# Performance work log

Measured on AMD Instinct MI355X. Metric: run time of the kernel, lower is better.

Reference implementation:

```python
import jax, jax.numpy as jnp
import numpy as np

DIM, HEADS, DHEAD, CTX_DIM, FF_MULT = 320, 8, 40, 768, 4
INNER_FF = FF_MULT * DIM  # 1280
EPS = 1e-5


def layer_norm(x, g, b):
    mu = jnp.mean(x, axis=-1, keepdims=True)
    var = jnp.mean((x - mu) ** 2, axis=-1, keepdims=True)
    return (x - mu) * jax.lax.rsqrt(var + EPS) * g + b


def attention(x, ctx, wq, wk, wv, wo, bo):
    # x: [b, i, DIM], ctx: [b, j, c]
    b, i, _ = x.shape
    j = ctx.shape[1]
    q = (x @ wq).reshape(b, i, HEADS, DHEAD)
    k = (ctx @ wk).reshape(b, j, HEADS, DHEAD)
    v = (ctx @ wv).reshape(b, j, HEADS, DHEAD)
    scale = DHEAD ** -0.5
    sim = jnp.einsum('bihd,bjhd->bhij', q, k) * scale  # full NxN, non-flash
    attn = jax.nn.softmax(sim, axis=-1)
    out = jnp.einsum('bhij,bjhd->bihd', attn, v).reshape(b, i, HEADS * DHEAD)
    return out @ wo + bo


def setup_inputs() -> dict:
    key = jax.random.key(0)
    ks = jax.random.split(key, 24)
    nrm = lambda k, shp, fan: jax.random.normal(k, shp, jnp.float32) * (fan ** -0.5)
    d = {
        'x': jax.random.normal(ks[0], (1, 4096, DIM), jnp.float32),
        'context': jax.random.normal(ks[1], (1, 77, CTX_DIM), jnp.float32),
        'n1_g': jnp.ones((DIM,), jnp.float32), 'n1_b': jnp.zeros((DIM,), jnp.float32),
        'a1_wq': nrm(ks[2], (DIM, DIM), DIM), 'a1_wk': nrm(ks[3], (DIM, DIM), DIM),
        'a1_wv': nrm(ks[4], (DIM, DIM), DIM), 'a1_wo': nrm(ks[5], (DIM, DIM), DIM),
        'a1_bo': jnp.zeros((DIM,), jnp.float32),
        'n2_g': jnp.ones((DIM,), jnp.float32), 'n2_b': jnp.zeros((DIM,), jnp.float32),
        'a2_wq': nrm(ks[6], (DIM, DIM), DIM), 'a2_wk': nrm(ks[7], (CTX_DIM, DIM), CTX_DIM),
        'a2_wv': nrm(ks[8], (CTX_DIM, DIM), CTX_DIM), 'a2_wo': nrm(ks[9], (DIM, DIM), DIM),
        'a2_bo': jnp.zeros((DIM,), jnp.float32),
        'n3_g': jnp.ones((DIM,), jnp.float32), 'n3_b': jnp.zeros((DIM,), jnp.float32),
        'ff_w1': nrm(ks[10], (DIM, 2 * INNER_FF), DIM),
        'ff_b1': jnp.zeros((2 * INNER_FF,), jnp.float32),
        'ff_w2': nrm(ks[11], (INNER_FF, DIM), INNER_FF),
        'ff_b2': jnp.zeros((DIM,), jnp.float32),
    }
    return d


def reference(x, context, n1_g, n1_b, a1_wq, a1_wk, a1_wv, a1_wo, a1_bo,
              n2_g, n2_b, a2_wq, a2_wk, a2_wv, a2_wo, a2_bo,
              n3_g, n3_b, ff_w1, ff_b1, ff_w2, ff_b2):
    # self-attention
    x = attention(layer_norm(x, n1_g, n1_b), layer_norm(x, n1_g, n1_b),
                  a1_wq, a1_wk, a1_wv, a1_wo, a1_bo) + x
    # cross-attention with text context
    x = attention(layer_norm(x, n2_g, n2_b), context,
                  a2_wq, a2_wk, a2_wv, a2_wo, a2_bo) + x
    # GEGLU feed-forward
    h = layer_norm(x, n3_g, n3_b) @ ff_w1 + ff_b1
    val, gate = jnp.split(h, 2, axis=-1)
    x = (val * jax.nn.gelu(gate, approximate=False)) @ ff_w2 + ff_b2 + x
    return x
```

## Files before the change

### kernel.cpp

```cpp
#include <hip/hip_runtime.h>
#include <hip/hip_bf16.h>
#include <math.h>

typedef __bf16 bf16;
typedef __attribute__((ext_vector_type(8))) __bf16 bf16x8;
typedef __attribute__((ext_vector_type(4))) __bf16 bf16x4;
typedef __attribute__((ext_vector_type(4))) float f32x4;
typedef __attribute__((ext_vector_type(2))) float f32x2;
typedef __attribute__((ext_vector_type(4))) short shortx4;

#define NTOK 4096
#define DIM  320
#define HEADS 8
#define DHEAD 40
#define NCTX 77
#define CTXD 768
#define IFF  1280

#define QSCALE (0.15811388300841897f * 1.4426950408889634f)

__device__ __forceinline__ bf16x8 bzero8() {
    bf16x8 v;
#pragma unroll
    for (int e = 0; e < 8; ++e) v[e] = (bf16)0.0f;
    return v;
}

__device__ __forceinline__ void gld_lds16(const void* g, void* l) {
    __builtin_amdgcn_global_load_lds(
        (const __attribute__((address_space(1))) void*)g,
        (__attribute__((address_space(3))) void*)l, 16, 0, 0);
}

__device__ __forceinline__ void ln_body(const float* __restrict__ X, const float* __restrict__ g,
                                        const float* __restrict__ b, bf16* __restrict__ Y, int row) {
    int lane = threadIdx.x & 63;
    const float* xr = X + (size_t)row * DIM;
    float v[5];
    float sum = 0.f;
#pragma unroll
    for (int c = 0; c < 5; ++c) { v[c] = xr[c * 64 + lane]; sum += v[c]; }
#pragma unroll
    for (int off = 1; off < 64; off <<= 1) sum += __shfl_xor(sum, off);
    float mu = sum * (1.f / 320.f);
    float vs = 0.f;
#pragma unroll
    for (int c = 0; c < 5; ++c) { float d = v[c] - mu; vs += d * d; }
#pragma unroll
    for (int off = 1; off < 64; off <<= 1) vs += __shfl_xor(vs, off);
    float rs = rsqrtf(vs * (1.f / 320.f) + 1e-5f);
    bf16* yr = Y + (size_t)row * DIM;
#pragma unroll
    for (int c = 0; c < 5; ++c)
        yr[c * 64 + lane] = (bf16)((v[c] - mu) * rs * g[c * 64 + lane] + b[c * 64 + lane]);
}

__global__ __launch_bounds__(256)
void layernorm_kernel(const float* __restrict__ X, const float* __restrict__ g,
                      const float* __restrict__ b, bf16* __restrict__ Y) {
    ln_body(X, g, b, Y, blockIdx.x * 4 + (threadIdx.x >> 6));
}

#define PRE_TILES 2280
#define CONV_BLOCKS 231
#define LN1_BLOCKS 1024

struct PreJob { const float* src; bf16* dst; int K, N, ntx, tile0, perm; };
struct PreTab { PreJob j[10]; };

__global__ __launch_bounds__(256)
void preprocess_all(PreTab P, const float* __restrict__ ctx, bf16* __restrict__ ctxb,
                    const float* __restrict__ x, const float* __restrict__ n1_g,
                    const float* __restrict__ n1_b, bf16* __restrict__ lnbuf) {
    const int b = blockIdx.x;
    const int t = threadIdx.x;
    if (b >= PRE_TILES + CONV_BLOCKS) {
        ln_body(x, n1_g, n1_b, lnbuf, (b - PRE_TILES - CONV_BLOCKS) * 4 + (t >> 6));
        return;
    }
    if (b >= PRE_TILES) {
        int i = (b - PRE_TILES) * 256 + t;
        if (i < NCTX * CTXD) ctxb[i] = (bf16)ctx[i];
        return;
    }
    const int tx = t & 31, ty = t >> 5;
    int ji = 0;
#pragma unroll
    for (int k = 1; k < 10; ++k)
        if (b >= P.j[k].tile0) ji = k;
    const PreJob jb = P.j[ji];
    const int local = b - jb.tile0;
    const int n0 = (local % jb.ntx) * 32;
    const int k0 = (local / jb.ntx) * 32;

    __shared__ float tile[32][33];
#pragma unroll
    for (int i = 0; i < 4; ++i)
        tile[ty + i * 8][tx] = jb.src[(size_t)(k0 + ty + i * 8) * jb.N + n0 + tx];
    __syncthreads();
#pragma unroll
    for (int i = 0; i < 4; ++i) {
        int n = n0 + ty + i * 8;
        int nd = jb.perm ? ((n < 1280) ? 2 * n : 2 * (n - 1280) + 1) : n;
        jb.dst[(size_t)nd * jb.K + k0 + tx] = (bf16)tile[tx][ty + i * 8];
    }
}

template <int EPI, int BM, int BN, int SWZ>
__global__ __launch_bounds__(256)
void gemm_db(const bf16* __restrict__ A, const bf16* __restrict__ Bt,
             int M, int N, int K,
             bf16* __restrict__ Y0, bf16* __restrict__ Y1, bf16* __restrict__ Y2,
             float* Yf, const float* __restrict__ bias, const float* res, int trs) {
    constexpr int ABYTES = BM * 128;
    constexpr int BBYTES = BN * 128;
    constexpr int FB = ABYTES + BBYTES;
    constexpr int WM = BM / 2;
    constexpr int WN = BN / 2;
    constexpr int MI = WM / 16;
    constexpr int NI = WN / 16;
    constexpr int ACH = BM / 32;
    constexpr int BCH = BN / 32;
    __shared__ char smem[2 * FB];
    const int t = threadIdx.x, lane = t & 63, w = t >> 6;
    const int wr = w >> 1, wc = w & 1;

    int bx = blockIdx.x, by = blockIdx.y;
    if (SWZ) {
        int gx = gridDim.x;
        int nwg = gx * gridDim.y;
        int bid = by * gx + bx;
        int s = (bid & 7) * (nwg >> 3) + (bid >> 3);
        bx = s % gx; by = s / gx;
    }
    const int m0 = bx * BM;
    const int n0 = by * BN;

    const bf16* asrc[ACH];
    const bf16* bsrc[BCH];
#pragma unroll
    for (int i = 0; i < ACH; ++i) {
        int ch = i * 256 + t;
        int row = ch >> 3, seg = (ch & 7) ^ (row & 7);
        asrc[i] = A + (size_t)(m0 + row) * K + seg * 8;
    }
#pragma unroll
    for (int i = 0; i < BCH; ++i) {
        int ch = i * 256 + t;
        int row = ch >> 3, seg = (ch & 7) ^ (row & 7);
        bsrc[i] = Bt + (size_t)(n0 + row) * K + seg * 8;
    }

    f32x4 acc[MI][NI];
#pragma unroll
    for (int mi = 0; mi < MI; ++mi)
#pragma unroll
        for (int ni = 0; ni < NI; ++ni)
#pragma unroll
            for (int r = 0; r < 4; ++r) acc[mi][ni][r] = 0.f;

    auto STAGE = [&](char* base, int k0) {
#pragma unroll
        for (int i = 0; i < ACH; ++i)
            gld_lds16(asrc[i] + k0, base + (i * 256 + w * 64) * 16);
#pragma unroll
        for (int i = 0; i < BCH; ++i)
            gld_lds16(bsrc[i] + k0, base + ABYTES + (i * 256 + w * 64) * 16);
    };

    char* cur = smem;
    char* nxt = smem + FB;
    STAGE(cur, 0);
    __syncthreads();

    for (int k0 = 0; k0 < K; k0 += 64) {
        if (k0 + 64 < K) STAGE(nxt, k0 + 64);
        bf16x8 a[MI][2], b[NI][2];
#pragma unroll
        for (int mi = 0; mi < MI; ++mi)
#pragma unroll
            for (int kh = 0; kh < 2; ++kh) {
                int row = wr * WM + mi * 16 + (lane & 15);
                a[mi][kh] = *(const bf16x8*)(cur + row * 128 +
                             ((kh * 64 + (lane >> 4) * 16) ^ ((row & 7) << 4)));
            }
#pragma unroll
        for (int ni = 0; ni < NI; ++ni)
#pragma unroll
            for (int kh = 0; kh < 2; ++kh) {
                int row = wc * WN + ni * 16 + (lane & 15);
                b[ni][kh] = *(const bf16x8*)(cur + ABYTES + row * 128 +
                             ((kh * 64 + (lane >> 4) * 16) ^ ((row & 7) << 4)));
            }
#pragma unroll
        for (int mi = 0; mi < MI; ++mi)
#pragma unroll
            for (int ni = 0; ni < NI; ++ni) {
                acc[mi][ni] = __builtin_amdgcn_mfma_f32_16x16x32_bf16(a[mi][0], b[ni][0], acc[mi][ni], 0, 0, 0);
                acc[mi][ni] = __builtin_amdgcn_mfma_f32_16x16x32_bf16(a[mi][1], b[ni][1], acc[mi][ni], 0, 0, 0);
            }
        __syncthreads();
        char* tmp = cur; cur = nxt; nxt = tmp;
    }

#pragma unroll
    for (int mi = 0; mi < MI; ++mi)
#pragma unroll
        for (int ni = 0; ni < NI; ++ni) {
            const int col = n0 + wc * WN + ni * 16 + (lane & 15);
            const int rowb = m0 + wr * WM + mi * 16 + (lane >> 4) * 4;
            if (EPI == 5) {
                if (col < 320) {
#pragma unroll
                    for (int r = 0; r < 4; ++r)
                        Y0[(size_t)(rowb + r) * 320 + col] = (bf16)(acc[mi][ni][r] * QSCALE);
                } else if (col < 640) {
#pragma unroll
                    for (int r = 0; r < 4; ++r)
                        Y1[(size_t)(rowb + r) * 320 + (col - 320)] = (bf16)acc[mi][ni][r];
                } else {
                    bf16x4 tv;
#pragma unroll
                    for (int r = 0; r < 4; ++r) tv[r] = (bf16)acc[mi][ni][r];
                    *(bf16x4*)(Y2 + (size_t)(col - 640) * trs + rowb) = tv;
                }
            } else if (EPI == 7) {
                int bidx = (col & 1) ? (1280 + (col >> 1)) : (col >> 1);
                float bc = bias[bidx];
#pragma unroll
                for (int r = 0; r < 4; ++r) {
                    float v = acc[mi][ni][r] + bc;
                    float other = __shfl_xor(v, 1);
                    if (!(col & 1)) {
                        float gl = 0.5f * other * (1.f + erff(other * 0.70710678118654752f));
                        Y0[(size_t)(rowb + r) * 1280 + (col >> 1)] = (bf16)(v * gl);
                    }
                }
            } else {
#pragma unroll
                for (int r = 0; r < 4; ++r) {
                    int row = rowb + r;
                    if (row < M) {
                        float v = acc[mi][ni][r];
                        if (EPI == 4) Y0[(size_t)row * N + col] = (bf16)(v * QSCALE);
                        else Yf[(size_t)row * N + col] = v + bias[col] + res[(size_t)row * N + col];
                    }
                }
            }
        }
}

__global__ __launch_bounds__(256)
void ln2_plus_cross(const float* __restrict__ X, const float* __restrict__ g,
                    const float* __restrict__ bb, bf16* __restrict__ Y,
                    const bf16* __restrict__ A, const bf16* __restrict__ Bt,
                    bf16* __restrict__ Y0, bf16* __restrict__ Y2, int trs) {
    __shared__ char smem[24 * 1024];
    if (blockIdx.x < 1024) {
        ln_body(X, g, bb, Y, blockIdx.x * 4 + (threadIdx.x >> 6));
        return;
    }
    const int M = NCTX, K = CTXD;
    const int t = threadIdx.x;
    const int lane = t & 63;
    const int w = t >> 6;
    const int wr = w >> 1, wc = w & 1;
    const int n0 = (blockIdx.x - 1024) * 64;

    f32x4 acc[4][2];
#pragma unroll
    for (int mi = 0; mi < 4; ++mi)
#pragma unroll
        for (int ni = 0; ni < 2; ++ni)
#pragma unroll
            for (int r = 0; r < 4; ++r) acc[mi][ni][r] = 0.f;

    for (int k0 = 0; k0 < K; k0 += 64) {
#pragma unroll
        for (int i = 0; i < 4; ++i) {
            int c = t + i * 256;
            int row = c >> 3, seg = c & 7;
            bf16x8 v = bzero8();
            if (row < M) v = *(const bf16x8*)(A + (size_t)row * K + k0 + seg * 8);
            *(bf16x8*)(smem + row * 128 + ((seg * 16) ^ ((row & 7) << 4))) = v;
        }
#pragma unroll
        for (int i = 0; i < 2; ++i) {
            int c = t + i * 256;
            int row = c >> 3, seg = c & 7;
            bf16x8 v = *(const bf16x8*)(Bt + (size_t)(n0 + row) * K + k0 + seg * 8);
            *(bf16x8*)(smem + 16 * 1024 + row * 128 + ((seg * 16) ^ ((row & 7) << 4))) = v;
        }
        __syncthreads();

        bf16x8 a[4][2], bfr[2][2];
#pragma unroll
        for (int mi = 0; mi < 4; ++mi)
#pragma unroll
            for (int kh = 0; kh < 2; ++kh) {
                int row = wr * 64 + mi * 16 + (lane & 15);
                a[mi][kh] = *(const bf16x8*)(smem + row * 128 +
                             ((kh * 64 + (lane >> 4) * 16) ^ ((row & 7) << 4)));
            }
#pragma unroll
        for (int ni = 0; ni < 2; ++ni)
#pragma unroll
            for (int kh = 0; kh < 2; ++kh) {
                int row = wc * 32 + ni * 16 + (lane & 15);
                bfr[ni][kh] = *(const bf16x8*)(smem + 16 * 1024 + row * 128 +
                               ((kh * 64 + (lane >> 4) * 16) ^ ((row & 7) << 4)));
            }
#pragma unroll
        for (int mi = 0; mi < 4; ++mi)
#pragma unroll
            for (int ni = 0; ni < 2; ++ni) {
                acc[mi][ni] = __builtin_amdgcn_mfma_f32_16x16x32_bf16(a[mi][0], bfr[ni][0], acc[mi][ni], 0, 0, 0);
                acc[mi][ni] = __builtin_amdgcn_mfma_f32_16x16x32_bf16(a[mi][1], bfr[ni][1], acc[mi][ni], 0, 0, 0);
            }
        __syncthreads();
    }

#pragma unroll
    for (int mi = 0; mi < 4; ++mi)
#pragma unroll
        for (int ni = 0; ni < 2; ++ni) {
            const int col = n0 + wc * 32 + ni * 16 + (lane & 15);
            const int rowb = wr * 64 + mi * 16 + (lane >> 4) * 4;
            if (col < 320) {
#pragma unroll
                for (int r = 0; r < 4; ++r)
                    if (rowb + r < M) Y0[(size_t)(rowb + r) * 320 + col] = (bf16)acc[mi][ni][r];
            } else {
                bf16x4 tv;
#pragma unroll
                for (int r = 0; r < 4; ++r) tv[r] = (bf16)acc[mi][ni][r];
                *(bf16x4*)(Y2 + (size_t)(col - 320) * trs + rowb) = tv;
            }
        }
}

#define KVT 64
#define KBYTES 5120
#define VBYTES 6144
#define FBUF (KBYTES + VBYTES)

template <int DIRECT>
__global__ __launch_bounds__(256, 4)
void flash_attn9(const bf16* __restrict__ Qg, const bf16* __restrict__ Kg,
                 const bf16* __restrict__ VTg, bf16* __restrict__ O,
                 bf16* __restrict__ Opart, float* __restrict__ MLpart,
                 int nkv, int vstride, int tiles_per_split) {
    __shared__ char smem[2 * FBUF];
    const int t = threadIdx.x, lane = t & 63, w = t >> 6;
    const int g = lane >> 4, q = lane & 15;
    const int h = blockIdx.y, split = blockIdx.z;
    const int qb = blockIdx.x * 64 + w * 16;

    const int ntiles = (nkv + KVT - 1) / KVT;
    const int tt0 = split * tiles_per_split;
    int tt1 = tt0 + tiles_per_split;
    if (tt1 > ntiles) tt1 = ntiles;

    if (t < 128) {
        bf16x8 v = bzero8();
        if (((t & 63) >> 3) == 0) {
#pragma unroll
            for (int e = 0; e < 8; ++e) v[e] = (bf16)1.0f;
        }
        *(bf16x8*)(smem + (t >> 6) * FBUF + KBYTES + 5120 + (t & 63) * 16) = v;
    }

    const int nslot = (w == 3) ? 1 : 3;
    const bf16* srcp[3];
    int dstoff[3], sstep[3];
#pragma unroll
    for (int s = 0; s < 3; ++s) {
        int id = w * 3 + s;
        if (id < 5) {
            int c16 = id * 64 + lane;
            int row = c16 / 5, seg = c16 - row * 5;
            srcp[s] = Kg + (size_t)(tt0 * KVT + row) * DIM + h * DHEAD + seg * 8;
            sstep[s] = KVT * DIM;
            dstoff[s] = id * 1024;
        } else {
            int vv = id - 5;
            int c16 = vv * 64 + lane;
            int row = c16 >> 3, seg = (c16 & 7) ^ (row & 7);
            srcp[s] = VTg + (size_t)(h * DHEAD + row) * vstride + tt0 * KVT + seg * 8;
            sstep[s] = KVT;
            dstoff[s] = KBYTES + vv * 1024;
        }
    }

#define STAGE(BUFOFF)                                                     \
    do {                                                                  \
        _Pragma("unroll")                                                 \
        for (int s = 0; s < 3; ++s) {                                     \
            if (s < nslot) {                                              \
                gld_lds16(srcp[s], smem + (BUFOFF) + dstoff[s]);          \
                srcp[s] += sstep[s];                                      \
            }                                                             \
        }                                                                 \
    } while (0)

    bf16x8 qf0 = *(const bf16x8*)(Qg + (size_t)(qb + q) * DIM + h * DHEAD + g * 8);
    bf16x8 qf1 = bzero8();
    if (g == 0) qf1 = *(const bf16x8*)(Qg + (size_t)(qb + q) * DIM + h * DHEAD + 32);

    f32x4 accO[3];
#pragma unroll
    for (int dt = 0; dt < 3; ++dt)
#pragma unroll
        for (int r = 0; r < 4; ++r) accO[dt][r] = 0.f;
    float m_run = -1e30f;

    const int swv = (q & 7) << 4;

#define TILE_BODY(KSC, J0)                                                        \
    do {                                                                          \
        const char* Ks_ = (KSC);                                                  \
        const char* Vs_ = Ks_ + KBYTES;                                           \
        const char* kb0b = Ks_ + q * 80 + g * 16;                                 \
        const char* kb1b = Ks_ + q * 80 + 64;                                     \
        f32x4 s4[4];                                                              \
        __builtin_amdgcn_s_setprio(1);                                            \
        _Pragma("unroll")                                                         \
        for (int jt = 0; jt < 4; ++jt) {                                          \
            bf16x8 kb0 = *(const bf16x8*)(kb0b + jt * 1280);                      \
            bf16x8 kb1 = *(const bf16x8*)(kb1b + jt * 1280);                      \
            f32x4 z;                                                              \
            _Pragma("unroll") for (int r = 0; r < 4; ++r) z[r] = 0.f;             \
            z = __builtin_amdgcn_mfma_f32_16x16x32_bf16(kb0, qf0, z, 0, 0, 0);    \
            z = __builtin_amdgcn_mfma_f32_16x16x32_bf16(kb1, qf1, z, 0, 0, 0);    \
            s4[jt] = z;                                                           \
        }                                                                         \
        __builtin_amdgcn_s_setprio(0);                                            \
        if ((J0) + KVT > nkv) {                                                   \
            _Pragma("unroll") for (int jt = 0; jt < 4; ++jt)                      \
            _Pragma("unroll") for (int r = 0; r < 4; ++r)                         \
                if ((J0) + jt * 16 + g * 4 + r >= nkv) s4[jt][r] = -1e30f;        \
        }                                                                         \
        float mvv0 = fmaxf(fmaxf(fmaxf(s4[0][0], s4[1][0]), s4[2][0]), s4[3][0]); \
        float mvv1 = fmaxf(fmaxf(fmaxf(s4[0][1], s4[1][1]), s4[2][1]), s4[3][1]); \
        float mvv2 = fmaxf(fmaxf(fmaxf(s4[0][2], s4[1][2]), s4[2][2]), s4[3][2]); \
        float mvv3 = fmaxf(fmaxf(fmaxf(s4[0][3], s4[1][3]), s4[2][3]), s4[3][3]); \
        float mt = fmaxf(fmaxf(fmaxf(mvv0, mvv1), mvv2), mvv3);                   \
        mt = fmaxf(mt, __shfl_xor(mt, 16));                                       \
        mt = fmaxf(mt, __shfl_xor(mt, 32));                                       \
        if (!__all(mt <= m_run + 8.f)) {                                          \
            float mnew = fmaxf(m_run, mt);                                        \
            float f = exp2f(m_run - mnew);                                        \
            m_run = mnew;                                                         \
            _Pragma("unroll") for (int dt = 0; dt < 3; ++dt)                      \
            _Pragma("unroll") for (int r = 0; r < 4; ++r) accO[dt][r] *= f;       \
        }                                                                         \
        union PU { bf16x4 hv; shortx4 sv; } pk[4];                                \
        _Pragma("unroll") for (int jt = 0; jt < 4; ++jt) {                        \
            bf16x4 hv;                                                            \
            _Pragma("unroll") for (int r = 0; r < 4; ++r)                         \
                hv[r] = (bf16)exp2f(s4[jt][r] - m_run);                           \
            pk[jt].hv = hv;                                                       \
        }                                                                         \
        __builtin_amdgcn_s_setprio(1);                                            \
        const char* vqb = Vs_ + q * 128;                                          \
        _Pragma("unroll") for (int jt = 0; jt < 4; ++jt) {                        \
            const char* vj = vqb + ((jt * 32 + g * 8) ^ swv);                     \
            _Pragma("unroll") for (int dt = 0; dt < 3; ++dt) {                    \
                shortx4 vb = *(const shortx4*)(vj + dt * 2048);                   \
                accO[dt] = __builtin_amdgcn_mfma_f32_16x16x16bf16_1k(             \
                               vb, pk[jt].sv, accO[dt], 0, 0, 0);                 \
            }                                                                     \
        }                                                                         \
        __builtin_amdgcn_s_setprio(0);                                            \
        __syncthreads();                                                          \
    } while (0)

    STAGE(0);
    __syncthreads();

    int tt = tt0;
    while (tt < tt1) {
        if (tt + 1 < tt1) STAGE(FBUF);
        TILE_BODY(smem, tt * KVT);
        ++tt;
        if (tt >= tt1) break;
        if (tt + 1 < tt1) STAGE(0);
        TILE_BODY(smem + FBUF, tt * KVT);
        ++tt;
    }
#undef TILE_BODY
#undef STAGE

    float l = __shfl(accO[2][0], 32 + q);

    if (DIRECT) {
        float inv = 1.f / l;
#pragma unroll
        for (int dt = 0; dt < 3; ++dt) {
            if (dt < 2 || g < 2) {
                bf16x4 o;
#pragma unroll
                for (int r = 0; r < 4; ++r) o[r] = (bf16)(accO[dt][r] * inv);
                *(bf16x4*)(O + (size_t)(qb + q) * DIM + h * DHEAD + dt * 16 + g * 4) = o;
            }
        }
    } else {
        size_t rowi = (size_t)(split * HEADS + h) * NTOK + qb + q;
#pragma unroll
        for (int dt = 0; dt < 3; ++dt) {
            if (dt < 2 || g < 2) {
                bf16x4 o;
#pragma unroll
                for (int r = 0; r < 4; ++r) o[r] = (bf16)accO[dt][r];
                *(bf16x4*)(Opart + rowi * 40 + dt * 16 + g * 4) = o;
            }
        }
        if (g == 2) {
            f32x2 ml;
            ml[0] = m_run; ml[1] = accO[2][0];
            *(f32x2*)(MLpart + rowi * 2) = ml;
        }
    }
}

__global__ __launch_bounds__(256)
void flash_combine(const bf16* __restrict__ Opart, const float* __restrict__ MLpart,
                   bf16* __restrict__ O) {
    int idx = blockIdx.x * 256 + threadIdx.x;
    int qi = idx / 40, c = idx - qi * 40;
    int h = c / 5, c8 = c - h * 5;
    float mv[4], lv[4];
    float M = -1e30f;
#pragma unroll
    for (int s = 0; s < 4; ++s) {
        f32x2 ml = *(const f32x2*)(MLpart + ((size_t)(s * HEADS + h) * NTOK + qi) * 2);
        mv[s] = ml[0]; lv[s] = ml[1];
        M = fmaxf(M, ml[0]);
    }
    float wgt[4], denom = 0.f;
#pragma unroll
    for (int s = 0; s < 4; ++s) { wgt[s] = exp2f(mv[s] - M); denom += wgt[s] * lv[s]; }
    float inv = 1.f / denom;
    float o[8];
#pragma unroll
    for (int e = 0; e < 8; ++e) o[e] = 0.f;
#pragma unroll
    for (int s = 0; s < 4; ++s) {
        bf16x8 op = *(const bf16x8*)(Opart + ((size_t)(s * HEADS + h) * NTOK + qi) * 40 + c8 * 8);
#pragma unroll
        for (int e = 0; e < 8; ++e) o[e] += wgt[s] * (float)op[e];
    }
    bf16x8 ov;
#pragma unroll
    for (int e = 0; e < 8; ++e) ov[e] = (bf16)(o[e] * inv);
    *(bf16x8*)(O + (size_t)qi * DIM + h * DHEAD + c8 * 8) = ov;
}

extern "C" void kernel_launch(void* const* d_in, const int* in_sizes, int n_in,
                              void* d_out, int out_size, void* d_ws, size_t ws_size,
                              hipStream_t stream) {
    const float* x     = (const float*)d_in[0];
    const float* ctx   = (const float*)d_in[1];
    const float* n1_g  = (const float*)d_in[2];
    const float* n1_b  = (const float*)d_in[3];
    const float* a1_wq = (const float*)d_in[4];
    const float* a1_wk = (const float*)d_in[5];
    const float* a1_wv = (const float*)d_in[6];
    const float* a1_wo = (const float*)d_in[7];
    const float* a1_bo = (const float*)d_in[8];
    const float* n2_g  = (const float*)d_in[9];
    const float* n2_b  = (const float*)d_in[10];
    const float* a2_wq = (const float*)d_in[11];
    const float* a2_wk = (const float*)d_in[12];
    const float* a2_wv = (const float*)d_in[13];
    const float* a2_wo = (const float*)d_in[14];
    const float* a2_bo = (const float*)d_in[15];
    const float* n3_g  = (const float*)d_in[16];
    const float* n3_b  = (const float*)d_in[17];
    const float* ff_w1 = (const float*)d_in[18];
    const float* ff_b1 = (const float*)d_in[19];
    const float* ff_w2 = (const float*)d_in[20];
    const float* ff_b2 = (const float*)d_in[21];

    char* ws = (char*)d_ws;
    size_t off = 0;
    auto alloc = [&](size_t bytes) -> char* {
        char* p = ws + off;
        off += (bytes + 255) & ~(size_t)255;
        return p;
    };
    bf16* lnbuf  = (bf16*)alloc((size_t)NTOK * DIM * 2);
    bf16* qbuf   = (bf16*)alloc((size_t)NTOK * DIM * 2);
    bf16* kbuf   = (bf16*)alloc((size_t)NTOK * DIM * 2);
    bf16* vtbuf  = (bf16*)alloc((size_t)DIM * NTOK * 2);
    bf16* abuf   = (bf16*)alloc((size_t)NTOK * DIM * 2);
    bf16* hbuf   = (bf16*)alloc((size_t)NTOK * 2 * IFF * 2);
    bf16* gbuf   = (bf16*)alloc((size_t)NTOK * IFF * 2);
    bf16* ctxb   = (bf16*)alloc((size_t)NCTX * CTXD * 2);
    bf16* k2buf  = (bf16*)alloc((size_t)128 * DIM * 2);
    bf16* vt2buf = (bf16*)alloc((size_t)DIM * 128 * 2);
    bf16* wqkvT  = (bf16*)alloc((size_t)960 * DIM * 2);
    bf16* woT    = (bf16*)alloc((size_t)DIM * DIM * 2);
    bf16* q2T    = (bf16*)alloc((size_t)DIM * DIM * 2);
    bf16* wkv2T  = (bf16*)alloc((size_t)640 * CTXD * 2);
    bf16* o2T    = (bf16*)alloc((size_t)DIM * DIM * 2);
    bf16* w1T    = (bf16*)alloc((size_t)2 * IFF * DIM * 2);
    bf16* w2T    = (bf16*)alloc((size_t)IFF * DIM * 2);
    float* out   = (float*)d_out;

    bf16*  Opart  = (bf16*)hbuf;
    float* MLpart = (float*)gbuf;

    {
        PreTab P;
        auto set = [&](int i, const float* s, bf16* d, int K, int N, int tile0, int perm) {
            P.j[i].src = s; P.j[i].dst = d; P.j[i].K = K; P.j[i].N = N;
            P.j[i].ntx = N / 32; P.j[i].tile0 = tile0; P.j[i].perm = perm;
        };
        set(0, a1_wq, wqkvT,                        320, 320,    0, 0);
        set(1, a1_wk, wqkvT + (size_t)320 * 320,    320, 320,  100, 0);
        set(2, a1_wv, wqkvT + (size_t)640 * 320,    320, 320,  200, 0);
        set(3, a1_wo, woT,                          320, 320,  300, 0);
        set(4, a2_wq, q2T,                          320, 320,  400, 0);
        set(5, a2_wo, o2T,                          320, 320,  500, 0);
        set(6, a2_wk, wkv2T,                        768, 320,  600, 0);
        set(7, a2_wv, wkv2T + (size_t)320 * 768,    768, 320,  840, 0);
        set(8, ff_w1, w1T,                          320, 2560, 1080, 1);
        set(9, ff_w2, w2T,                          1280, 320, 1880, 0);
        preprocess_all<<<PRE_TILES + CONV_BLOCKS + LN1_BLOCKS, 256, 0, stream>>>(
            P, ctx, ctxb, x, n1_g, n1_b, lnbuf);
    }

    gemm_db<5, 128, 64, 1><<<dim3(32, 15), 256, 0, stream>>>(lnbuf, wqkvT, NTOK, 960, DIM,
                                                             qbuf, kbuf, vtbuf, nullptr, nullptr, nullptr, NTOK);
    flash_attn9<0><<<dim3(64, 8, 4), 256, 0, stream>>>(qbuf, kbuf, vtbuf, nullptr,
                                                       Opart, MLpart, NTOK, NTOK, 16);
    flash_combine<<<640, 256, 0, stream>>>(Opart, MLpart, abuf);
    gemm_db<2, 64, 64, 1><<<dim3(64, 5), 256, 0, stream>>>(abuf, woT, NTOK, DIM, DIM,
                                                           nullptr, nullptr, nullptr, out, a1_bo, x, 0);

    ln2_plus_cross<<<1034, 256, 0, stream>>>(out, n2_g, n2_b, lnbuf,
                                             ctxb, wkv2T, k2buf, vt2buf, 128);
    gemm_db<4, 64, 64, 1><<<dim3(64, 5), 256, 0, stream>>>(lnbuf, q2T, NTOK, DIM, DIM,
                                                           qbuf, nullptr, nullptr, nullptr, nullptr, nullptr, 0);
    flash_attn9<1><<<dim3(64, 8, 1), 256, 0, stream>>>(qbuf, k2buf, vt2buf, abuf,
                                                       nullptr, nullptr, NCTX, 128, 2);
    gemm_db<2, 64, 64, 1><<<dim3(64, 5), 256, 0, stream>>>(abuf, o2T, NTOK, DIM, DIM,
                                                           nullptr, nullptr, nullptr, out, a2_bo, out, 0);

    layernorm_kernel<<<1024, 256, 0, stream>>>(out, n3_g, n3_b, lnbuf);
    gemm_db<7, 128, 64, 1><<<dim3(32, 40), 256, 0, stream>>>(lnbuf, w1T, NTOK, 2 * IFF, DIM,
                                                             gbuf, nullptr, nullptr, nullptr, ff_b1, nullptr, 0);
    gemm_db<2, 64, 64, 1><<<dim3(64, 5), 256, 0, stream>>>(gbuf, w2T, NTOK, DIM, IFF,
                                                           nullptr, nullptr, nullptr, out, ff_b2, out, 0);
}
```

Baseline: 179.7 us.

## Process two query tiles per wave in flash attention to reuse K/V loads

Result: slower. 186.4 us (+3.8%).

```diff
diff --git a/kernel.cpp b/kernel.cpp
--- a/kernel.cpp
+++ b/kernel.cpp
@@ -346,15 +346,16 @@
 
 template <int DIRECT>
 __global__ __launch_bounds__(256, 4)
-void flash_attn9(const bf16* __restrict__ Qg, const bf16* __restrict__ Kg,
-                 const bf16* __restrict__ VTg, bf16* __restrict__ O,
-                 bf16* __restrict__ Opart, float* __restrict__ MLpart,
-                 int nkv, int vstride, int tiles_per_split) {
+void flash_attn10(const bf16* __restrict__ Qg, const bf16* __restrict__ Kg,
+                  const bf16* __restrict__ VTg, bf16* __restrict__ O,
+                  bf16* __restrict__ Opart, float* __restrict__ MLpart,
+                  int nkv, int vstride, int tiles_per_split) {
     __shared__ char smem[2 * FBUF];
     const int t = threadIdx.x, lane = t & 63, w = t >> 6;
     const int g = lane >> 4, q = lane & 15;
     const int h = blockIdx.y, split = blockIdx.z;
-    const int qb = blockIdx.x * 64 + w * 16;
+    const int qbA = blockIdx.x * 128 + w * 16;
+    const int qbB = qbA + 64;
 
     const int ntiles = (nkv + KVT - 1) / KVT;
     const int tt0 = split * tiles_per_split;
@@ -403,16 +404,20 @@
         }                                                                 \
     } while (0)
 
-    bf16x8 qf0 = *(const bf16x8*)(Qg + (size_t)(qb + q) * DIM + h * DHEAD + g * 8);
-    bf16x8 qf1 = bzero8();
-    if (g == 0) qf1 = *(const bf16x8*)(Qg + (size_t)(qb + q) * DIM + h * DHEAD + 32);
-
-    f32x4 accO[3];
+    bf16x8 qf0a = *(const bf16x8*)(Qg + (size_t)(qbA + q) * DIM + h * DHEAD + g * 8);
+    bf16x8 qf0b = *(const bf16x8*)(Qg + (size_t)(qbB + q) * DIM + h * DHEAD + g * 8);
+    bf16x8 qf1a = bzero8(), qf1b = bzero8();
+    if (g == 0) {
+        qf1a = *(const bf16x8*)(Qg + (size_t)(qbA + q) * DIM + h * DHEAD + 32);
+        qf1b = *(const bf16x8*)(Qg + (size_t)(qbB + q) * DIM + h * DHEAD + 32);
+    }
+
+    f32x4 accA[3], accB[3];
 #pragma unroll
     for (int dt = 0; dt < 3; ++dt)
 #pragma unroll
-        for (int r = 0; r < 4; ++r) accO[dt][r] = 0.f;
-    float m_run = -1e30f;
+        for (int r = 0; r < 4; ++r) { accA[dt][r] = 0.f; accB[dt][r] = 0.f; }
+    float mA = -1e30f, mB = -1e30f;
 
     const int swv = (q & 7) << 4;
 
@@ -422,44 +427,66 @@
         const char* Vs_ = Ks_ + KBYTES;                                           \
         const char* kb0b = Ks_ + q * 80 + g * 16;                                 \
         const char* kb1b = Ks_ + q * 80 + 64;                                     \
-        f32x4 s4[4];                                                              \
+        f32x4 sa[4], sb[4];                                                       \
         __builtin_amdgcn_s_setprio(1);                                            \
         _Pragma("unroll")                                                         \
         for (int jt = 0; jt < 4; ++jt) {                                          \
             bf16x8 kb0 = *(const bf16x8*)(kb0b + jt * 1280);                      \
             bf16x8 kb1 = *(const bf16x8*)(kb1b + jt * 1280);                      \
-            f32x4 z;                                                              \
-            _Pragma("unroll") for (int r = 0; r < 4; ++r) z[r] = 0.f;             \
-            z = __builtin_amdgcn_mfma_f32_16x16x32_bf16(kb0, qf0, z, 0, 0, 0);    \
-            z = __builtin_amdgcn_mfma_f32_16x16x32_bf16(kb1, qf1, z, 0, 0, 0);    \
-            s4[jt] = z;                                                           \
+            f32x4 za, zb;                                                         \
+            _Pragma("unroll") for (int r = 0; r < 4; ++r) { za[r] = 0.f; zb[r] = 0.f; } \
+            za = __builtin_amdgcn_mfma_f32_16x16x32_bf16(kb0, qf0a, za, 0, 0, 0); \
+            za = __builtin_amdgcn_mfma_f32_16x16x32_bf16(kb1, qf1a, za, 0, 0, 0); \
+            zb = __builtin_amdgcn_mfma_f32_16x16x32_bf16(kb0, qf0b, zb, 0, 0, 0); \
+            zb = __builtin_amdgcn_mfma_f32_16x16x32_bf16(kb1, qf1b, zb, 0, 0, 0); \
+            sa[jt] = za; sb[jt] = zb;                                             \
         }                                                                         \
         __builtin_amdgcn_s_setprio(0);                                            \
         if ((J0) + KVT > nkv) {                                                   \
             _Pragma("unroll") for (int jt = 0; jt < 4; ++jt)                      \
             _Pragma("unroll") for (int r = 0; r < 4; ++r)                         \
-                if ((J0) + jt * 16 + g * 4 + r >= nkv) s4[jt][r] = -1e30f;        \
+                if ((J0) + jt * 16 + g * 4 + r >= nkv) { sa[jt][r] = -1e30f; sb[jt][r] = -1e30f; } \
         }                                                                         \
-        float mvv0 = fmaxf(fmaxf(fmaxf(s4[0][0], s4[1][0]), s4[2][0]), s4[3][0]); \
-        float mvv1 = fmaxf(fmaxf(fmaxf(s4[0][1], s4[1][1]), s4[2][1]), s4[3][1]); \
-        float mvv2 = fmaxf(fmaxf(fmaxf(s4[0][2], s4[1][2]), s4[2][2]), s4[3][2]); \
-        float mvv3 = fmaxf(fmaxf(fmaxf(s4[0][3], s4[1][3]), s4[2][3]), s4[3][3]); \
-        float mt = fmaxf(fmaxf(fmaxf(mvv0, mvv1), mvv2), mvv3);                   \
-        mt = fmaxf(mt, __shfl_xor(mt, 16));                                       \
-        mt = fmaxf(mt, __shfl_xor(mt, 32));                                       \
-        if (!__all(mt <= m_run + 8.f)) {                                          \
-            float mnew = fmaxf(m_run, mt);                                        \
-            float f = exp2f(m_run - mnew);                                        \
-            m_run = mnew;                                                         \
-            _Pragma("unroll") for (int dt = 0; dt < 3; ++dt)                      \
-            _Pragma("unroll") for (int r = 0; r < 4; ++r) accO[dt][r] *= f;       \
+        {                                                                         \
+            float m0_ = fmaxf(fmaxf(fmaxf(sa[0][0], sa[1][0]), sa[2][0]), sa[3][0]); \
+            float m1_ = fmaxf(fmaxf(fmaxf(sa[0][1], sa[1][1]), sa[2][1]), sa[3][1]); \
+            float m2_ = fmaxf(fmaxf(fmaxf(sa[0][2], sa[1][2]), sa[2][2]), sa[3][2]); \
+            float m3_ = fmaxf(fmaxf(fmaxf(sa[0][3], sa[1][3]), sa[2][3]), sa[3][3]); \
+            float mt = fmaxf(fmaxf(fmaxf(m0_, m1_), m2_), m3_);                   \
+            mt = fmaxf(mt, __shfl_xor(mt, 16));                                   \
+            mt = fmaxf(mt, __shfl_xor(mt, 32));                                   \
+            if (!__all(mt <= mA + 8.f)) {                                         \
+                float mnew = fmaxf(mA, mt);                                       \
+                float f = exp2f(mA - mnew);                                       \
+                mA = mnew;                                                        \
+                _Pragma("unroll") for (int dt = 0; dt < 3; ++dt)                  \
+                _Pragma("unroll") for (int r = 0; r < 4; ++r) accA[dt][r] *= f;   \
+            }                                                                     \
         }                                                                         \
-        union PU { bf16x4 hv; shortx4 sv; } pk[4];                                \
+        {                                                                         \
+            float m0_ = fmaxf(fmaxf(fmaxf(sb[0][0], sb[1][0]), sb[2][0]), sb[3][0]); \
+            float m1_ = fmaxf(fmaxf(fmaxf(sb[0][1], sb[1][1]), sb[2][1]), sb[3][1]); \
+            float m2_ = fmaxf(fmaxf(fmaxf(sb[0][2], sb[1][2]), sb[2][2]), sb[3][2]); \
+            float m3_ = fmaxf(fmaxf(fmaxf(sb[0][3], sb[1][3]), sb[2][3]), sb[3][3]); \
+            float mt = fmaxf(fmaxf(fmaxf(m0_, m1_), m2_), m3_);                   \
+            mt = fmaxf(mt, __shfl_xor(mt, 16));                                   \
+            mt = fmaxf(mt, __shfl_xor(mt, 32));                                   \
+            if (!__all(mt <= mB + 8.f)) {                                         \
+                float mnew = fmaxf(mB, mt);                                       \
+                float f = exp2f(mB - mnew);                                       \
+                mB = mnew;                                                        \
+                _Pragma("unroll") for (int dt = 0; dt < 3; ++dt)                  \
+                _Pragma("unroll") for (int r = 0; r < 4; ++r) accB[dt][r] *= f;   \
+            }                                                                     \
+        }                                                                         \
+        union PU { bf16x4 hv; shortx4 sv; } pkA[4], pkB[4];                       \
         _Pragma("unroll") for (int jt = 0; jt < 4; ++jt) {                        \
-            bf16x4 hv;                                                            \
-            _Pragma("unroll") for (int r = 0; r < 4; ++r)                         \
-                hv[r] = (bf16)exp2f(s4[jt][r] - m_run);                           \
-            pk[jt].hv = hv;                                                       \
+            bf16x4 ha, hb;                                                        \
+            _Pragma("unroll") for (int r = 0; r < 4; ++r) {                       \
+                ha[r] = (bf16)exp2f(sa[jt][r] - mA);                              \
+                hb[r] = (bf16)exp2f(sb[jt][r] - mB);                              \
+            }                                                                     \
+            pkA[jt].hv = ha; pkB[jt].hv = hb;                                     \
         }                                                                         \
         __builtin_amdgcn_s_setprio(1);                                            \
         const char* vqb = Vs_ + q * 128;                                          \
@@ -467,8 +494,10 @@
             const char* vj = vqb + ((jt * 32 + g * 8) ^ swv);                     \
             _Pragma("unroll") for (int dt = 0; dt < 3; ++dt) {                    \
                 shortx4 vb = *(const shortx4*)(vj + dt * 2048);                   \
-                accO[dt] = __builtin_amdgcn_mfma_f32_16x16x16bf16_1k(             \
-                               vb, pk[jt].sv, accO[dt], 0, 0, 0);                 \
+                accA[dt] = __builtin_amdgcn_mfma_f32_16x16x16bf16_1k(             \
+                               vb, pkA[jt].sv, accA[dt], 0, 0, 0);                \
+                accB[dt] = __builtin_amdgcn_mfma_f32_16x16x16bf16_1k(             \
+                               vb, pkB[jt].sv, accB[dt], 0, 0, 0);                \
             }                                                                     \
         }                                                                         \
         __builtin_amdgcn_s_setprio(0);                                            \
@@ -491,34 +520,45 @@
 #undef TILE_BODY
 #undef STAGE
 
-    float l = __shfl(accO[2][0], 32 + q);
+    float lA = __shfl(accA[2][0], 32 + q);
+    float lB = __shfl(accB[2][0], 32 + q);
 
     if (DIRECT) {
-        float inv = 1.f / l;
+        float invA = 1.f / lA, invB = 1.f / lB;
 #pragma unroll
         for (int dt = 0; dt < 3; ++dt) {
             if (dt < 2 || g < 2) {
-                bf16x4 o;
-#pragma unroll
-                for (int r = 0; r < 4; ++r) o[r] = (bf16)(accO[dt][r] * inv);
-                *(bf16x4*)(O + (size_t)(qb + q) * DIM + h * DHEAD + dt * 16 + g * 4) = o;
+                bf16x4 oa, ob;
+#pragma unroll
+                for (int r = 0; r < 4; ++r) {
+                    oa[r] = (bf16)(accA[dt][r] * invA);
+                    ob[r] = (bf16)(accB[dt][r] * invB);
+                }
+                *(bf16x4*)(O + (size_t)(qbA + q) * DIM + h * DHEAD + dt * 16 + g * 4) = oa;
+                *(bf16x4*)(O + (size_t)(qbB + q) * DIM + h * DHEAD + dt * 16 + g * 4) = ob;
             }
         }
     } else {
-        size_t rowi = (size_t)(split * HEADS + h) * NTOK + qb + q;
+        size_t rowA = (size_t)(split * HEADS + h) * NTOK + qbA + q;
+        size_t rowB = rowA + 64;
 #pragma unroll
         for (int dt = 0; dt < 3; ++dt) {
             if (dt < 2 || g < 2) {
-                bf16x4 o;
-#pragma unroll
-                for (int r = 0; r < 4; ++r) o[r] = (bf16)accO[dt][r];
-                *(bf16x4*)(Opart + rowi * 40 + dt * 16 + g * 4) = o;
+                bf16x4 oa, ob;
+#pragma unroll
+                for (int r = 0; r < 4; ++r) {
+                    oa[r] = (bf16)accA[dt][r];
+                    ob[r] = (bf16)accB[dt][r];
+                }
+                *(bf16x4*)(Opart + rowA * 40 + dt * 16 + g * 4) = oa;
+                *(bf16x4*)(Opart + rowB * 40 + dt * 16 + g * 4) = ob;
             }
         }
         if (g == 2) {
-            f32x2 ml;
-            ml[0] = m_run; ml[1] = accO[2][0];
-            *(f32x2*)(MLpart + rowi * 2) = ml;
+            f32x2 mla; mla[0] = mA; mla[1] = accA[2][0];
+            f32x2 mlb; mlb[0] = mB; mlb[1] = accB[2][0];
+            *(f32x2*)(MLpart + rowA * 2) = mla;
+            *(f32x2*)(MLpart + rowB * 2) = mlb;
         }
     }
 }
@@ -633,8 +673,8 @@
 
     gemm_db<5, 128, 64, 1><<<dim3(32, 15), 256, 0, stream>>>(lnbuf, wqkvT, NTOK, 960, DIM,
                                                              qbuf, kbuf, vtbuf, nullptr, nullptr, nullptr, NTOK);
-    flash_attn9<0><<<dim3(64, 8, 4), 256, 0, stream>>>(qbuf, kbuf, vtbuf, nullptr,
-                                                       Opart, MLpart, NTOK, NTOK, 16);
+    flash_attn10<0><<<dim3(32, 8, 4), 256, 0, stream>>>(qbuf, kbuf, vtbuf, nullptr,
+                                                        Opart, MLpart, NTOK, NTOK, 16);
     flash_combine<<<640, 256, 0, stream>>>(Opart, MLpart, abuf);
     gemm_db<2, 64, 64, 1><<<dim3(64, 5), 256, 0, stream>>>(abuf, woT, NTOK, DIM, DIM,
                                                            nullptr, nullptr, nullptr, out, a1_bo, x, 0);
@@ -643,8 +683,8 @@
                                              ctxb, wkv2T, k2buf, vt2buf, 128);
     gemm_db<4, 64, 64, 1><<<dim3(64, 5), 256, 0, stream>>>(lnbuf, q2T, NTOK, DIM, DIM,
                                                            qbuf, nullptr, nullptr, nullptr, nullptr, nullptr, 0);
-    flash_attn9<1><<<dim3(64, 8, 1), 256, 0, stream>>>(qbuf, k2buf, vt2buf, abuf,
-                                                       nullptr, nullptr, NCTX, 128, 2);
+    flash_attn10<1><<<dim3(32, 8, 1), 256, 0, stream>>>(qbuf, k2buf, vt2buf, abuf,
+                                                        nullptr, nullptr, NCTX, 128, 2);
     gemm_db<2, 64, 64, 1><<<dim3(64, 5), 256, 0, stream>>>(abuf, o2T, NTOK, DIM, DIM,
                                                            nullptr, nullptr, nullptr, out, a2_bo, out, 0);
 
```
